# Kernel optimization log

Measured on AMD Instinct MI355X. Metric: run time of the kernel, lower is better.

Reference implementation:

```python
import jax, jax.numpy as jnp
import numpy as np

DIM = 2048
K = 4  # num_components


def setup_inputs() -> dict:
    key = jax.random.key(0)
    k1, k2, k3, k4 = jax.random.split(key, 4)
    x = jax.random.normal(k1, (2, 4096, DIM), dtype=jnp.float32)
    means = jax.random.normal(k2, (1, 1, K, 2), dtype=jnp.float32)
    # inv_var_covar initialized as A @ A^T (PSD), matching torch init
    A = jax.random.normal(k3, (K, 2, 2), dtype=jnp.float32)
    inv_var_covar = jnp.einsum('kij,klj->kil', A, A)
    # log(softplus(randn)) init, matching torch
    log_weights = jnp.log(jax.nn.softplus(
        jax.random.normal(k4, (1, 1, 1, K, 2), dtype=jnp.float32)))
    return {"x": x, "means": means, "inv_var_covar": inv_var_covar,
            "log_weights": log_weights}


def gmm2d(x, means, inv_var_covar, log_weights):
    B, S, D = x.shape
    xr = x.astype(jnp.float32).reshape(B, S, D // 2, 2)
    # diff: [B, S, P, K, 2] where P = D//2
    diff = xr[:, :, :, None, :] - means[0, 0]
    # quadratic form per 2x2 component: [B, S, P, K]
    log_g = -0.5 * jnp.einsum('bspki,kij,bspkj->bspk',
                              diff, inv_var_covar, diff)
    max_log = jnp.max(log_g, axis=-1, keepdims=True)  # [B,S,P,1]
    # add per-component per-output log weights: [B,S,P,K,2]
    w = log_g[..., None] + log_weights[0, 0, 0] - max_log[..., None]
    lse = jax.nn.logsumexp(w, axis=-2) + max_log      # [B,S,P,2]
    return jnp.exp(lse).reshape(B, S, D)


def reference(x, means, inv_var_covar, log_weights):
    return x * gmm2d(x, means, inv_var_covar, log_weights)
```

## Files before the change

### kernel.cpp

```cpp
#include <hip/hip_runtime.h>
#include <hip/hip_bf16.h>


__global__ __launch_bounds__(256) void gmm2d_act_kernel(
    const float4* __restrict__ x,
    const float*  __restrict__ means,
    const float*  __restrict__ ivc,
    const float*  __restrict__ lw,
    float4* __restrict__ out,
    int n4)
{
    float m0[4], m1[4], Aq[4], Bq[4], Cq[4], W0[4], W1[4];
#pragma unroll
    for (int k = 0; k < 4; ++k) {
        m0[k] = means[2*k + 0];
        m1[k] = means[2*k + 1];
        Aq[k] = -0.5f *  ivc[4*k + 0];
        Bq[k] = -0.5f * (ivc[4*k + 1] + ivc[4*k + 2]);
        Cq[k] = -0.5f *  ivc[4*k + 3];
        W0[k] = expf(lw[2*k + 0]);
        W1[k] = expf(lw[2*k + 1]);
    }

    const int stride = gridDim.x * blockDim.x;
    for (int i = blockIdx.x * blockDim.x + threadIdx.x; i < n4; i += stride) {
        float4 v = x[i];
        float r0, r1, r2, r3;
        {
            float s0 = 0.f, s1 = 0.f;
#pragma unroll
            for (int k = 0; k < 4; ++k) {
                float d0 = v.x - m0[k];
                float d1 = v.y - m1[k];
                float q  = Aq[k]*d0*d0 + Bq[k]*d0*d1 + Cq[k]*d1*d1;
                float e  = __expf(q);
                s0 = fmaf(e, W0[k], s0);
                s1 = fmaf(e, W1[k], s1);
            }
            r0 = v.x * s0;
            r1 = v.y * s1;
        }
        {
            float s0 = 0.f, s1 = 0.f;
#pragma unroll
            for (int k = 0; k < 4; ++k) {
                float d0 = v.z - m0[k];
                float d1 = v.w - m1[k];
                float q  = Aq[k]*d0*d0 + Bq[k]*d0*d1 + Cq[k]*d1*d1;
                float e  = __expf(q);
                s0 = fmaf(e, W0[k], s0);
                s1 = fmaf(e, W1[k], s1);
            }
            r2 = v.z * s0;
            r3 = v.w * s1;
        }
        out[i] = make_float4(r0, r1, r2, r3);
    }
}

extern "C" void kernel_launch(void* const* d_in, const int* in_sizes, int n_in,
                              void* d_out, int out_size, void* d_ws, size_t ws_size,
                              hipStream_t stream) {
    const float4* x   = (const float4*)d_in[0];
    const float* means = (const float*)d_in[1];
    const float* ivc   = (const float*)d_in[2];
    const float* lw    = (const float*)d_in[3];
    float4* out = (float4*)d_out;

    const int n4 = out_size / 4;
    const int block = 256;
    const int grid = 2048;

    gmm2d_act_kernel<<<grid, block, 0, stream>>>(x, means, ivc, lw, out, n4);
}
```

Before: 26.90 us.

## Batch loads per thread, use native exp2, nontemporal stores

```diff
diff --git a/kernel.cpp b/kernel.cpp
--- a/kernel.cpp
+++ b/kernel.cpp
@@ -2,12 +2,17 @@
 #include <hip/hip_bf16.h>
 
 
+#define LOG2E 1.4426950408889634f
+
+typedef float f32x4 __attribute__((ext_vector_type(4)));
+
+template <int ITERS>
 __global__ __launch_bounds__(256) void gmm2d_act_kernel(
-    const float4* __restrict__ x,
-    const float*  __restrict__ means,
-    const float*  __restrict__ ivc,
-    const float*  __restrict__ lw,
-    float4* __restrict__ out,
+    const f32x4* __restrict__ x,
+    const float* __restrict__ means,
+    const float* __restrict__ ivc,
+    const float* __restrict__ lw,
+    f32x4* __restrict__ out,
     int n4)
 {
     float m0[4], m1[4], Aq[4], Bq[4], Cq[4], W0[4], W1[4];
@@ -15,61 +20,87 @@
     for (int k = 0; k < 4; ++k) {
         m0[k] = means[2*k + 0];
         m1[k] = means[2*k + 1];
-        Aq[k] = -0.5f *  ivc[4*k + 0];
-        Bq[k] = -0.5f * (ivc[4*k + 1] + ivc[4*k + 2]);
-        Cq[k] = -0.5f *  ivc[4*k + 3];
+        Aq[k] = -0.5f * LOG2E *  ivc[4*k + 0];
+        Bq[k] = -0.5f * LOG2E * (ivc[4*k + 1] + ivc[4*k + 2]);
+        Cq[k] = -0.5f * LOG2E *  ivc[4*k + 3];
         W0[k] = expf(lw[2*k + 0]);
         W1[k] = expf(lw[2*k + 1]);
     }
 
     const int stride = gridDim.x * blockDim.x;
-    for (int i = blockIdx.x * blockDim.x + threadIdx.x; i < n4; i += stride) {
-        float4 v = x[i];
-        float r0, r1, r2, r3;
-        {
-            float s0 = 0.f, s1 = 0.f;
+    const int tid = blockIdx.x * blockDim.x + threadIdx.x;
+
+    if (ITERS * stride == n4 || tid + (ITERS - 1) * stride < n4) {
+        f32x4 v[ITERS];
 #pragma unroll
-            for (int k = 0; k < 4; ++k) {
-                float d0 = v.x - m0[k];
-                float d1 = v.y - m1[k];
-                float q  = Aq[k]*d0*d0 + Bq[k]*d0*d1 + Cq[k]*d1*d1;
-                float e  = __expf(q);
-                s0 = fmaf(e, W0[k], s0);
-                s1 = fmaf(e, W1[k], s1);
+        for (int it = 0; it < ITERS; ++it)
+            v[it] = x[tid + it * stride];
+
+#pragma unroll
+        for (int it = 0; it < ITERS; ++it) {
+            f32x4 r;
+#pragma unroll
+            for (int p = 0; p < 2; ++p) {
+                float x0 = v[it][2*p + 0];
+                float x1 = v[it][2*p + 1];
+                float s0 = 0.f, s1 = 0.f;
+#pragma unroll
+                for (int k = 0; k < 4; ++k) {
+                    float d0 = x0 - m0[k];
+                    float d1 = x1 - m1[k];
+                    float t  = fmaf(Bq[k], d1, Aq[k] * d0);
+                    float q  = fmaf(Cq[k] * d1, d1, d0 * t);
+                    float e  = __builtin_amdgcn_exp2f(q);
+                    s0 = fmaf(e, W0[k], s0);
+                    s1 = fmaf(e, W1[k], s1);
+                }
+                r[2*p + 0] = x0 * s0;
+                r[2*p + 1] = x1 * s1;
             }
-            r0 = v.x * s0;
-            r1 = v.y * s1;
+            __builtin_nontemporal_store(r, &out[tid + it * stride]);
         }
-        {
-            float s0 = 0.f, s1 = 0.f;
+    } else {
+        for (int i = tid; i < n4; i += stride) {
+            f32x4 v = x[i];
+            f32x4 r;
 #pragma unroll
-            for (int k = 0; k < 4; ++k) {
-                float d0 = v.z - m0[k];
-                float d1 = v.w - m1[k];
-                float q  = Aq[k]*d0*d0 + Bq[k]*d0*d1 + Cq[k]*d1*d1;
-                float e  = __expf(q);
-                s0 = fmaf(e, W0[k], s0);
-                s1 = fmaf(e, W1[k], s1);
+            for (int p = 0; p < 2; ++p) {
+                float x0 = v[2*p + 0];
+                float x1 = v[2*p + 1];
+                float s0 = 0.f, s1 = 0.f;
+#pragma unroll
+                for (int k = 0; k < 4; ++k) {
+                    float d0 = x0 - m0[k];
+                    float d1 = x1 - m1[k];
+                    float t  = fmaf(Bq[k], d1, Aq[k] * d0);
+                    float q  = fmaf(Cq[k] * d1, d1, d0 * t);
+                    float e  = __builtin_amdgcn_exp2f(q);
+                    s0 = fmaf(e, W0[k], s0);
+                    s1 = fmaf(e, W1[k], s1);
+                }
+                r[2*p + 0] = x0 * s0;
+                r[2*p + 1] = x1 * s1;
             }
-            r2 = v.z * s0;
-            r3 = v.w * s1;
+            __builtin_nontemporal_store(r, &out[i]);
         }
-        out[i] = make_float4(r0, r1, r2, r3);
     }
 }
 
 extern "C" void kernel_launch(void* const* d_in, const int* in_sizes, int n_in,
                               void* d_out, int out_size, void* d_ws, size_t ws_size,
                               hipStream_t stream) {
-    const float4* x   = (const float4*)d_in[0];
+    const f32x4* x     = (const f32x4*)d_in[0];
     const float* means = (const float*)d_in[1];
     const float* ivc   = (const float*)d_in[2];
     const float* lw    = (const float*)d_in[3];
-    float4* out = (float4*)d_out;
+    f32x4* out = (f32x4*)d_out;
 
     const int n4 = out_size / 4;
     const int block = 256;
-    const int grid = 2048;
 
-    gmm2d_act_kernel<<<grid, block, 0, stream>>>(x, means, ivc, lw, out, n4);
+    if (n4 % (4096 * block * 4) == 0) {
+        gmm2d_act_kernel<4><<<4096, block, 0, stream>>>(x, means, ivc, lw, out, n4);
+    } else {
+        gmm2d_act_kernel<1><<<(n4 + block - 1) / block, block, 0, stream>>>(x, means, ivc, lw, out, n4);
+    }
 }
```

After: 26.57 us. No clear change (-1.2%).
